# Kernel tuning notes

Measured on AMD Instinct MI355X. Metric: run time of the kernel, lower is better.

Reference implementation:

```python
import jax, jax.numpy as jnp
import numpy as np

NUM_HEADS = 8
DIM_HEAD = 64
SCALE = DIM_HEAD * NUM_HEADS  # q *= dim_head * num_heads, as in the source


def setup_inputs() -> dict:
    key = jax.random.key(0)
    k1, k2, k3, k4 = jax.random.split(key, 4)
    B, C, H, W = 8, 64, 32, 32
    x = jax.random.normal(k1, (B, C, H, W), dtype=jnp.float32)
    # 1x1 conv == matmul over channels; small init keeps post-scale logits sane
    w_qkv = jax.random.normal(k2, (3 * NUM_HEADS * DIM_HEAD, C), dtype=jnp.float32) * 0.02
    rel_h = jax.random.normal(k3, (2 * H - 1, DIM_HEAD), dtype=jnp.float32) * 0.02
    rel_w = jax.random.normal(k4, (2 * W - 1, DIM_HEAD), dtype=jnp.float32) * 0.02
    return {"x": x, "w_qkv": w_qkv, "rel_h": rel_h, "rel_w": rel_w}


def _rel_indices(H, W):
    # flattened 2D grid positions
    pos_y = np.repeat(np.arange(H), W)  # [HW]
    pos_x = np.tile(np.arange(W), H)    # [HW]
    rel_y = pos_y[None, :] - pos_y[:, None] + (H - 1)  # [HW, HW] in [0, 2H-2]
    rel_x = pos_x[None, :] - pos_x[:, None] + (W - 1)  # [HW, HW] in [0, 2W-2]
    return jnp.asarray(rel_y), jnp.asarray(rel_x)


def reference(x, w_qkv, rel_h, rel_w):
    B, C, H, W = x.shape
    n = H * W
    # 1x1 conv (bias=False) -> per-pixel matmul
    xf = x.reshape(B, C, n)                              # b c n
    qkv = jnp.einsum('oc,bcn->bon', w_qkv, xf)           # b (3 h d) n
    q, k, v = jnp.split(qkv, 3, axis=1)
    def to_heads(t):  # b (h d) n -> b h n d
        return t.reshape(B, NUM_HEADS, DIM_HEAD, n).transpose(0, 1, 3, 2)
    q, k, v = to_heads(q), to_heads(k), to_heads(v)
    q = q * SCALE  # scale applied before QK^T AND before pos bias (in-place in torch)

    sim = jnp.einsum('bhid,bhjd->bhij', q, k)            # [B, h, n, n]

    # relative position bias: q_i . rel_h[dy] + q_i . rel_w[dx]
    logits_h = jnp.einsum('bhid,rd->bhir', q, rel_h)     # [B, h, n, 2H-1]
    logits_w = jnp.einsum('bhid,rd->bhir', q, rel_w)     # [B, h, n, 2W-1]
    rel_y, rel_x = _rel_indices(H, W)                    # [n, n] each
    i_idx = jnp.arange(n)[:, None]                       # [n, 1]
    bias = logits_h[:, :, i_idx, rel_y] + logits_w[:, :, i_idx, rel_x]  # [B,h,n,n]

    attn = jax.nn.softmax(sim + bias, axis=-1)
    out = jnp.einsum('bhij,bhjd->bhid', attn, v)         # [B, h, n, d]
    out = out.transpose(0, 1, 3, 2).reshape(B, NUM_HEADS * DIM_HEAD, H, W)
    return out
```

## Files before the change

kernel.cpp:

```cpp
#include <hip/hip_runtime.h>
#include <hip/hip_bf16.h>
#include <hip/hip_fp16.h>

typedef _Float16 h8 __attribute__((ext_vector_type(8)));
typedef _Float16 h2 __attribute__((ext_vector_type(2)));
typedef unsigned short us8 __attribute__((ext_vector_type(8)));
typedef float f4 __attribute__((ext_vector_type(4)));
typedef float f16v __attribute__((ext_vector_type(16)));
typedef int i2v __attribute__((ext_vector_type(2)));

#define NH 8
#define DH 64
#define NPIX 1024
#define CIN 64
#define NBH 64
#define QSCALE (512.0f * 1.44269504f)
#define LOSCALE 2048.0f
#define INV_LOSCALE (1.0f / 2048.0f)
#define DTHR 12.0f

__device__ __forceinline__ void gload_lds16(const void* g, void* lds) {
  __builtin_amdgcn_global_load_lds(
      (const __attribute__((address_space(1))) void*)g,
      (__attribute__((address_space(3))) void*)lds, 16, 0, 0);
}

__device__ __forceinline__ float fexp2(float x) {
#if __has_builtin(__builtin_amdgcn_exp2f)
  return __builtin_amdgcn_exp2f(x);
#else
  return exp2f(x);
#endif
}

__device__ __forceinline__ unsigned pk16(float a, float b) {
  auto r = __builtin_amdgcn_cvt_pkrtz(a, b);
  union { decltype(r) h; unsigned u; } x;
  x.h = r;
  return x.u;
}

__global__ __launch_bounds__(256) void qkv_mfma(
    const float* __restrict__ x, const float* __restrict__ wqkv,
    _Float16* __restrict__ Qh, _Float16* __restrict__ Ql,
    _Float16* __restrict__ Kh, _Float16* __restrict__ Kl,
    _Float16* __restrict__ Vv) {
  __shared__ __align__(16) char QS[49152];
  char* Wh = QS;
  char* Wl = QS + 16384;
  char* Xh = QS + 32768;
  char* Xl = QS + 40960;
  char* Thi = QS;
  char* Tlo = QS + 16384;

  const int tid = threadIdx.x;
  const int lane = tid & 63;
  const int w = tid >> 6;
  const int c = lane & 15;
  const int g = lane >> 4;
  const int o0 = blockIdx.x * 128;
  const int p0 = blockIdx.y * 64;
  const int b = blockIdx.z;

  #pragma unroll
  for (int it = 0; it < 4; ++it) {
    int task = tid + it * 256;
    int oct = task & 7, o = task >> 3;
    const f4* wr = (const f4*)(wqkv + (size_t)(o0 + o) * CIN + oct * 8);
    f4 wa = wr[0], wb = wr[1];
    h8 hi, lo;
    #pragma unroll
    for (int e = 0; e < 8; ++e) {
      float v = e < 4 ? wa[e] : wb[e - 4];
      _Float16 h = (_Float16)v;
      hi[e] = h;
      lo[e] = (_Float16)((v - (float)h) * LOSCALE);
    }
    int byo = o * 128 + ((oct ^ (o & 7)) << 4);
    *(h8*)(Wh + byo) = hi;
    *(h8*)(Wl + byo) = lo;
  }
  {
    int kp = tid & 31;
    int pgrp = tid >> 5;
    const float* xr0 = x + ((size_t)b * CIN + 2 * kp) * NPIX + p0 + pgrp * 8;
    const float* xr1 = xr0 + NPIX;
    f4 a0 = *(const f4*)xr0, a1 = *(const f4*)(xr0 + 4);
    f4 b0 = *(const f4*)xr1, b1 = *(const f4*)(xr1 + 4);
    int oct = kp >> 2;
    int slot4 = (kp & 3) * 4;
    #pragma unroll
    for (int e = 0; e < 8; ++e) {
      float v0 = e < 4 ? a0[e] : a1[e - 4];
      float v1 = e < 4 ? b0[e] : b1[e - 4];
      _Float16 h0 = (_Float16)v0, h1 = (_Float16)v1;
      float l0f = (v0 - (float)h0) * LOSCALE;
      float l1f = (v1 - (float)h1) * LOSCALE;
      int p = pgrp * 8 + e;
      int byo = p * 128 + ((oct ^ (p & 7)) << 4) + slot4;
      union { h2 h; unsigned u; } uh, ul;
      uh.h[0] = h0; uh.h[1] = h1;
      ul.h[0] = (_Float16)l0f; ul.h[1] = (_Float16)l1f;
      *(unsigned*)(Xh + byo) = uh.u;
      *(unsigned*)(Xl + byo) = ul.u;
    }
  }
  __syncthreads();

  f4 zf = {0.f, 0.f, 0.f, 0.f};
  f4 acc[2][4], cor[2][4];
  #pragma unroll
  for (int oi = 0; oi < 2; ++oi)
    #pragma unroll
    for (int pi = 0; pi < 4; ++pi) { acc[oi][pi] = zf; cor[oi][pi] = zf; }

  const int ob = w * 32;
  #pragma unroll
  for (int kh = 0; kh < 2; ++kh) {
    h8 ah[2], al[2], bh[4], bl[4];
    #pragma unroll
    for (int oi = 0; oi < 2; ++oi) {
      int orow = ob + ((c >> 2) << 3) + (c & 3) + oi * 4;
      int ch = (((kh * 4 + g) ^ (orow & 7)) << 4);
      ah[oi] = *(const h8*)(Wh + orow * 128 + ch);
      al[oi] = *(const h8*)(Wl + orow * 128 + ch);
    }
    #pragma unroll
    for (int pi = 0; pi < 4; ++pi) {
      int prow = pi * 16 + c;
      int ch = (((kh * 4 + g) ^ (prow & 7)) << 4);
      bh[pi] = *(const h8*)(Xh + prow * 128 + ch);
      bl[pi] = *(const h8*)(Xl + prow * 128 + ch);
    }
    __builtin_amdgcn_s_setprio(1);
    #pragma unroll
    for (int oi = 0; oi < 2; ++oi)
      #pragma unroll
      for (int pi = 0; pi < 4; ++pi) {
        acc[oi][pi] = __builtin_amdgcn_mfma_f32_16x16x32_f16(ah[oi], bh[pi], acc[oi][pi], 0, 0, 0);
        cor[oi][pi] = __builtin_amdgcn_mfma_f32_16x16x32_f16(ah[oi], bl[pi], cor[oi][pi], 0, 0, 0);
        cor[oi][pi] = __builtin_amdgcn_mfma_f32_16x16x32_f16(al[oi], bh[pi], cor[oi][pi], 0, 0, 0);
      }
    __builtin_amdgcn_s_setprio(0);
  }

  const int part = o0 >> 9;
  const float scl = part == 0 ? QSCALE : 1.0f;
  _Float16* dsth = part == 0 ? Qh : (part == 1 ? Kh : Vv);
  _Float16* dstl = part == 0 ? Ql : (part == 1 ? Kl : nullptr);

  __syncthreads();
  {
    const int chunk = 4 * w + g;
    #pragma unroll
    for (int pi = 0; pi < 4; ++pi) {
      int p = pi * 16 + c;
      h8 hv, lv;
      #pragma unroll
      for (int oi = 0; oi < 2; ++oi)
        #pragma unroll
        for (int reg = 0; reg < 4; ++reg) {
          float v = (acc[oi][pi][reg] + cor[oi][pi][reg] * INV_LOSCALE) * scl;
          _Float16 hh = (_Float16)v;
          hv[oi * 4 + reg] = hh;
          lv[oi * 4 + reg] = (_Float16)(v - (float)hh);
        }
      int byo = p * 256 + ((chunk ^ (p & 15)) << 4);
      *(h8*)(Thi + byo) = hv;
      if (dstl) *(h8*)(Tlo + byo) = lv;
    }
  }
  __syncthreads();
  #pragma unroll
  for (int it = 0; it < 4; ++it) {
    int task = tid + it * 256;
    int p = task >> 4;
    int ck = task & 15;
    int byo = p * 256 + ((ck ^ (p & 15)) << 4);
    int o = o0 + ck * 8;
    int h = (o >> 6) & 7;
    int d = o & 63;
    size_t off = (((size_t)(b * NH + h)) * NPIX + p0 + p) * DH + d;
    h8 v = *(const h8*)(Thi + byo);
    *(h8*)(dsth + off) = v;
    if (dstl) {
      h8 v2 = *(const h8*)(Tlo + byo);
      *(h8*)(dstl + off) = v2;
    }
  }
}

__global__ __launch_bounds__(256, 2) void attn_mfma(
    const _Float16* __restrict__ Qh, const _Float16* __restrict__ Ql,
    const _Float16* __restrict__ Kh, const _Float16* __restrict__ Kl,
    const _Float16* __restrict__ V,
    const float* __restrict__ rel_h, const float* __restrict__ rel_w,
    float* __restrict__ out) {
  __shared__ __align__(16) char SMem[57344];
  _Float16* LHc = (_Float16*)(SMem + 49152);
  _Float16* LWT = (_Float16*)(SMem + 32768);
  float* OT = (float*)SMem;

  const int tid = threadIdx.x;
  const int lane = tid & 63;
  const int w = tid >> 6;
  const int wu = __builtin_amdgcn_readfirstlane(w);
  const int c = lane & 15;
  const int g = lane >> 4;
  const int il = lane & 31;
  const int hi = lane >> 5;
  const int bx = blockIdx.x;
  const int bh = ((bx & 7) << 3) | ((bx >> 3) & 7);
  const int i0 = (bx >> 6) << 7;

  const _Float16* Qhg = Qh + (size_t)bh * NPIX * DH;
  const _Float16* Qlg = Ql + (size_t)bh * NPIX * DH;
  const _Float16* Khg = Kh + (size_t)bh * NPIX * DH;
  const _Float16* Klg = Kl + (size_t)bh * NPIX * DH;
  const _Float16* Vg  = V  + (size_t)bh * NPIX * DH;

  const h8* Qr0h = (const h8*)(Qhg + (size_t)(i0 + w * 32 + c) * DH);
  const h8* Qr0l = (const h8*)(Qlg + (size_t)(i0 + w * 32 + c) * DH);
  const h8* Qr1h = (const h8*)(Qhg + (size_t)(i0 + w * 32 + 16 + c) * DH);
  const h8* Qr1l = (const h8*)(Qlg + (size_t)(i0 + w * 32 + 16 + c) * DH);
  h8 q0h[2] = {Qr0h[g], Qr0h[4 + g]};
  h8 q0l[2] = {Qr0l[g], Qr0l[4 + g]};
  h8 q1h[2] = {Qr1h[g], Qr1h[4 + g]};
  h8 q1l[2] = {Qr1l[g], Qr1l[4 + g]};

  const int s0i = wu * 128 + lane;
  const int s1i = s0i + 64;
  const int ko0 = (s0i >> 3) * 128 + (((s0i & 7) ^ ((s0i >> 3) & 7)) << 4);
  const int ko1 = (s1i >> 3) * 128 + (((s1i & 7) ^ ((s1i >> 3) & 7)) << 4);

  #pragma unroll
  for (int it = 0; it < 2; ++it) {
    int task = tid + it * 256;
    int oct = task & 7, s = task >> 3;
    int ss = s < 63 ? s : 62;
    const float* sh = rel_h + (size_t)ss * DH + oct * 8;
    const float* sw = rel_w + (size_t)ss * DH + oct * 8;
    h8 hh, ww;
    #pragma unroll
    for (int e = 0; e < 8; ++e) {
      hh[e] = (_Float16)sh[e];
      ww[e] = (_Float16)sw[e];
    }
    int byo = s * 128 + ((oct ^ (s & 7)) << 4);
    *(h8*)(SMem + byo) = hh;
    *(h8*)(SMem + 16384 + byo) = ww;
  }
  __syncthreads();

  const int yi = (i0 + w * 32) >> 5;
  f4 zf = {0.f, 0.f, 0.f, 0.f};
  #pragma unroll
  for (int rs = 0; rs < 2; ++rs) {
    f4 lhD[4], lwD[4];
    #pragma unroll
    for (int st = 0; st < 4; ++st) { lhD[st] = zf; lwD[st] = zf; }
    #pragma unroll
    for (int kh = 0; kh < 2; ++kh) {
      h8 bq = rs ? q1h[kh] : q0h[kh];
      h8 bl = rs ? q1l[kh] : q0l[kh];
      #pragma unroll
      for (int st = 0; st < 4; ++st) {
        int srow = st * 16 + c;
        int chb = srow * 128 + (((kh * 4 + g) ^ (srow & 7)) << 4);
        h8 ra = *(const h8*)(SMem + chb);
        h8 wa = *(const h8*)(SMem + 16384 + chb);
        lhD[st] = __builtin_amdgcn_mfma_f32_16x16x32_f16(ra, bq, lhD[st], 0, 0, 0);
        lhD[st] = __builtin_amdgcn_mfma_f32_16x16x32_f16(ra, bl, lhD[st], 0, 0, 0);
        lwD[st] = __builtin_amdgcn_mfma_f32_16x16x32_f16(wa, bq, lwD[st], 0, 0, 0);
        lwD[st] = __builtin_amdgcn_mfma_f32_16x16x32_f16(wa, bl, lwD[st], 0, 0, 0);
      }
    }
    int lrow = w * 32 + rs * 16 + c;
    #pragma unroll
    for (int st = 0; st < 4; ++st)
      #pragma unroll
      for (int reg = 0; reg < 4; ++reg) {
        int s = st * 16 + 4 * g + reg;
        int k = s - 31 + yi;
        if (k >= 0 && k < 32)
          LHc[(k >> 1) * 256 + lrow * 2 + (k & 1)] = (_Float16)lhD[st][reg];
        LWT[lrow * 64 + s] = (_Float16)lwD[st][reg];
      }
  }
  __syncthreads();

  float lwp[16];
  {
    int r = w * 32 + il;
    #pragma unroll
    for (int reg = 0; reg < 16; ++reg) {
      int jl = (reg & 3) + 8 * (reg >> 2) + 4 * hi;
      lwp[reg] = (float)LWT[r * 64 + 31 + jl - il];
    }
  }
  const h8* Qmh = (const h8*)(Qhg + (size_t)(i0 + w * 32 + il) * DH);
  const h8* Qml = (const h8*)(Qlg + (size_t)(i0 + w * 32 + il) * DH);
  h8 qmh[4], qml[4];
  #pragma unroll
  for (int kb = 0; kb < 4; ++kb) {
    qmh[kb] = Qmh[2 * kb + hi];
    qml[kb] = Qml[2 * kb + hi];
  }
  __syncthreads();

  {
    gload_lds16((const char*)Khg + ko0, SMem + wu * 2048);
    gload_lds16((const char*)Khg + ko1, SMem + wu * 2048 + 1024);
    gload_lds16((const char*)Klg + ko0, SMem + 16384 + wu * 2048);
    gload_lds16((const char*)Klg + ko1, SMem + 16384 + wu * 2048 + 1024);
    int jp = tid & 31, dd = tid >> 5;
    const h8* vr = (const h8*)(Vg + (size_t)(2 * jp) * DH);
    h8 v0 = vr[dd], v1 = vr[8 + dd];
    us8 u0 = *(const us8*)&v0, u1 = *(const us8*)&v1;
    #pragma unroll
    for (int e = 0; e < 8; ++e) {
      int d = dd * 8 + e;
      unsigned int val = (unsigned int)u0[e] | ((unsigned int)u1[e] << 16);
      *(unsigned int*)(SMem + 32768 + d * 128 + (((jp >> 2) ^ (d & 7)) << 4) + (jp & 3) * 4) = val;
    }
  }
  __syncthreads();

  float m_s = -1e30f, lp = 0.f;
  f16v O0, O1;
  #pragma unroll
  for (int e = 0; e < 16; ++e) { O0[e] = 0.f; O1[e] = 0.f; }

  const int swl = (il & 7);
  int cur = 0;
  #pragma unroll 1
  for (int t = 0; t < 16; ++t) {
    char* Kc  = SMem + cur * 8192;
    char* KLc = SMem + 16384 + cur * 8192;
    char* Vc  = SMem + 32768 + cur * 8192;
    const int nxt = cur ^ 1;
    const bool pre = t < 15;
    const int jp = tid & 31, dd = tid >> 5;
    h8 v0 = {}, v1 = {};
    if (pre) {
      const char* kg  = (const char*)Khg + (size_t)(t + 1) * 8192;
      const char* klg = (const char*)Klg + (size_t)(t + 1) * 8192;
      gload_lds16(kg + ko0, SMem + nxt * 8192 + wu * 2048);
      gload_lds16(kg + ko1, SMem + nxt * 8192 + wu * 2048 + 1024);
      gload_lds16(klg + ko0, SMem + 16384 + nxt * 8192 + wu * 2048);
      gload_lds16(klg + ko1, SMem + 16384 + nxt * 8192 + wu * 2048 + 1024);
      const h8* vr = (const h8*)(Vg + (size_t)((t + 1) * 64 + 2 * jp) * DH);
      v0 = vr[dd];
      v1 = vr[8 + dd];
    }

    f16v S0, S1;
    #pragma unroll
    for (int e = 0; e < 16; ++e) { S0[e] = 0.f; S1[e] = 0.f; }
    #pragma unroll
    for (int kb = 0; kb < 4; ++kb) {
      int chb0 = il * 128 + (((2 * kb + hi) ^ swl) << 4);
      int chb1 = chb0 + 32 * 128;
      h8 a0h = *(const h8*)(Kc + chb0);
      h8 a0l = *(const h8*)(KLc + chb0);
      h8 a1h = *(const h8*)(Kc + chb1);
      h8 a1l = *(const h8*)(KLc + chb1);
      __builtin_amdgcn_s_setprio(1);
      S0 = __builtin_amdgcn_mfma_f32_32x32x16_f16(a0h, qmh[kb], S0, 0, 0, 0);
      S0 = __builtin_amdgcn_mfma_f32_32x32x16_f16(a0l, qmh[kb], S0, 0, 0, 0);
      S0 = __builtin_amdgcn_mfma_f32_32x32x16_f16(a0h, qml[kb], S0, 0, 0, 0);
      S1 = __builtin_amdgcn_mfma_f32_32x32x16_f16(a1h, qmh[kb], S1, 0, 0, 0);
      S1 = __builtin_amdgcn_mfma_f32_32x32x16_f16(a1l, qmh[kb], S1, 0, 0, 0);
      S1 = __builtin_amdgcn_mfma_f32_32x32x16_f16(a1h, qml[kb], S1, 0, 0, 0);
      __builtin_amdgcn_s_setprio(0);
    }

    h8 fr[4];
    {
      int r = w * 32 + il;
      h2 lhu = *(const h2*)(LHc + t * 256 + r * 2);
      float lh0 = (float)lhu[0], lh1 = (float)lhu[1];
      #pragma unroll
      for (int reg = 0; reg < 16; ++reg) {
        S0[reg] += lwp[reg] + lh0;
        S1[reg] += lwp[reg] + lh1;
      }
      float pv0[16], pv1[16];
      #pragma unroll
      for (int e = 0; e < 16; ++e) {
        pv0[e] = fexp2(S0[e] - m_s);
        pv1[e] = fexp2(S1[e] - m_s);
      }
      float v8[8];
      #pragma unroll
      for (int e = 0; e < 8; ++e)
        v8[e] = fmaxf(fmaxf(S0[e], S0[e + 8]), fmaxf(S1[e], S1[e + 8]));
      float w0 = fmaxf(fmaxf(v8[0], v8[1]), fmaxf(v8[2], v8[3]));
      float w1 = fmaxf(fmaxf(v8[4], v8[5]), fmaxf(v8[6], v8[7]));
      float mx = fmaxf(w0, w1);
      mx = fmaxf(mx, __shfl_xor(mx, 32, 64));
      bool sk = mx <= m_s + DTHR;
      if (!__all(sk)) {
        float mn = fmaxf(m_s, mx);
        float corr = fexp2(m_s - mn);
        m_s = mn;
        lp *= corr;
        #pragma unroll
        for (int e = 0; e < 16; ++e) { O0[e] *= corr; O1[e] *= corr; }
        #pragma unroll
        for (int e = 0; e < 16; ++e) {
          pv0[e] = fexp2(S0[e] - m_s);
          pv1[e] = fexp2(S1[e] - m_s);
        }
      }
      f4 ps = zf;
      #pragma unroll
      for (int e = 0; e < 16; e += 4) {
        ps[0] += pv0[e] + pv1[e];
        ps[1] += pv0[e + 1] + pv1[e + 1];
        ps[2] += pv0[e + 2] + pv1[e + 2];
        ps[3] += pv0[e + 3] + pv1[e + 3];
      }
      lp += (ps[0] + ps[1]) + (ps[2] + ps[3]);
      #pragma unroll
      for (int jkb = 0; jkb < 4; ++jkb) {
        const float* pv = (jkb < 2) ? pv0 : pv1;
        int base = (jkb & 1) * 8;
        unsigned x01 = pk16(pv[base + 0], pv[base + 1]);
        unsigned x23 = pk16(pv[base + 2], pv[base + 3]);
        unsigned y01 = pk16(pv[base + 4], pv[base + 5]);
        unsigned y23 = pk16(pv[base + 6], pv[base + 7]);
        i2v r1 = __builtin_amdgcn_permlane32_swap((int)x01, (int)y01, false, false);
        i2v r2 = __builtin_amdgcn_permlane32_swap((int)x23, (int)y23, false, false);
        union { unsigned u[4]; h8 h; } fu;
        fu.u[0] = (unsigned)r1[0];
        fu.u[1] = (unsigned)r2[0];
        fu.u[2] = (unsigned)r1[1];
        fu.u[3] = (unsigned)r2[1];
        fr[jkb] = fu.h;
      }
    }

    #pragma unroll
    for (int jkb = 0; jkb < 4; ++jkb) {
      int och = (((2 * jkb + hi) ^ swl) << 4);
      __builtin_amdgcn_s_setprio(1);
      h8 av0 = *(const h8*)(Vc + il * 128 + och);
      h8 av1 = *(const h8*)(Vc + (32 + il) * 128 + och);
      O0 = __builtin_amdgcn_mfma_f32_32x32x16_f16(av0, fr[jkb], O0, 0, 0, 0);
      O1 = __builtin_amdgcn_mfma_f32_32x32x16_f16(av1, fr[jkb], O1, 0, 0, 0);
      __builtin_amdgcn_s_setprio(0);
    }

    if (pre) {
      us8 u0 = *(const us8*)&v0, u1 = *(const us8*)&v1;
      char* Vn = SMem + 32768 + nxt * 8192;
      #pragma unroll
      for (int e = 0; e < 8; ++e) {
        int d = dd * 8 + e;
        unsigned int val = (unsigned int)u0[e] | ((unsigned int)u1[e] << 16);
        *(unsigned int*)(Vn + d * 128 + (((jp >> 2) ^ (d & 7)) << 4) + (jp & 3) * 4) = val;
      }
    }
    __syncthreads();
    cur = nxt;
  }

  float lt = lp + __shfl_xor(lp, 32, 64);
  float rr = __builtin_amdgcn_rcpf(lt);
  {
    int r = w * 32 + il;
    #pragma unroll
    for (int reg = 0; reg < 16; ++reg) {
      int dl = (reg & 3) + 8 * (reg >> 2) + 4 * hi;
      int d0 = dl;
      int d1 = 32 + dl;
      OT[d0 * 128 + (r ^ ((d0 & 7) << 3))] = O0[reg] * rr;
      OT[d1 * 128 + (r ^ ((d1 & 7) << 3))] = O1[reg] * rr;
    }
  }
  __syncthreads();
  #pragma unroll
  for (int it = 0; it < 8; ++it) {
    int task = tid + it * 256;
    int rq = task & 31, d = task >> 5;
    f4 vv = *(const f4*)&OT[d * 128 + ((rq * 4) ^ ((d & 7) << 3))];
    *(f4*)(out + (((size_t)bh * 64 + d) << 10) + i0 + rq * 4) = vv;
  }
}

extern "C" void kernel_launch(void* const* d_in, const int* in_sizes, int n_in,
                              void* d_out, int out_size, void* d_ws, size_t ws_size,
                              hipStream_t stream) {
  const float* x  = (const float*)d_in[0];
  const float* wq = (const float*)d_in[1];
  const float* rh = (const float*)d_in[2];
  const float* rw = (const float*)d_in[3];
  float* out = (float*)d_out;

  const size_t sz = (size_t)NBH * NPIX * DH;
  _Float16* Qh = (_Float16*)d_ws;
  _Float16* Ql = Qh + sz;
  _Float16* Kh = Ql + sz;
  _Float16* Kl = Kh + sz;
  _Float16* V  = Kl + sz;

  qkv_mfma<<<dim3(12, 16, 8), 256, 0, stream>>>(x, wq, Qh, Ql, Kh, Kl, V);
  attn_mfma<<<dim3(512), 256, 0, stream>>>(Qh, Ql, Kh, Kl, V, rh, rw, out);
}
```

Measured before the change: 72.07 us.

## Store V transposed and load K/V fragments directly from global instead of LDS

```diff
diff --git a/kernel.cpp b/kernel.cpp
--- a/kernel.cpp
+++ b/kernel.cpp
@@ -4,7 +4,6 @@
 
 typedef _Float16 h8 __attribute__((ext_vector_type(8)));
 typedef _Float16 h2 __attribute__((ext_vector_type(2)));
-typedef unsigned short us8 __attribute__((ext_vector_type(8)));
 typedef float f4 __attribute__((ext_vector_type(4)));
 typedef float f16v __attribute__((ext_vector_type(16)));
 typedef int i2v __attribute__((ext_vector_type(2)));
@@ -19,12 +18,6 @@
 #define INV_LOSCALE (1.0f / 2048.0f)
 #define DTHR 12.0f
 
-__device__ __forceinline__ void gload_lds16(const void* g, void* lds) {
-  __builtin_amdgcn_global_load_lds(
-      (const __attribute__((address_space(1))) void*)g,
-      (__attribute__((address_space(3))) void*)lds, 16, 0, 0);
-}
-
 __device__ __forceinline__ float fexp2(float x) {
 #if __has_builtin(__builtin_amdgcn_exp2f)
   return __builtin_amdgcn_exp2f(x);
@@ -44,7 +37,7 @@
     const float* __restrict__ x, const float* __restrict__ wqkv,
     _Float16* __restrict__ Qh, _Float16* __restrict__ Ql,
     _Float16* __restrict__ Kh, _Float16* __restrict__ Kl,
-    _Float16* __restrict__ Vv) {
+    _Float16* __restrict__ Vt) {
   __shared__ __align__(16) char QS[49152];
   char* Wh = QS;
   char* Wl = QS + 16384;
@@ -146,7 +139,7 @@
 
   const int part = o0 >> 9;
   const float scl = part == 0 ? QSCALE : 1.0f;
-  _Float16* dsth = part == 0 ? Qh : (part == 1 ? Kh : Vv);
+  _Float16* dsth = part == 0 ? Qh : (part == 1 ? Kh : Vt);
   _Float16* dstl = part == 0 ? Ql : (part == 1 ? Kl : nullptr);
 
   __syncthreads();
@@ -171,40 +164,59 @@
     }
   }
   __syncthreads();
-  #pragma unroll
-  for (int it = 0; it < 4; ++it) {
-    int task = tid + it * 256;
-    int p = task >> 4;
-    int ck = task & 15;
-    int byo = p * 256 + ((ck ^ (p & 15)) << 4);
-    int o = o0 + ck * 8;
-    int h = (o >> 6) & 7;
-    int d = o & 63;
-    size_t off = (((size_t)(b * NH + h)) * NPIX + p0 + p) * DH + d;
-    h8 v = *(const h8*)(Thi + byo);
-    *(h8*)(dsth + off) = v;
-    if (dstl) {
-      h8 v2 = *(const h8*)(Tlo + byo);
-      *(h8*)(dstl + off) = v2;
+  if (part != 2) {
+    #pragma unroll
+    for (int it = 0; it < 4; ++it) {
+      int task = tid + it * 256;
+      int p = task >> 4;
+      int ck = task & 15;
+      int byo = p * 256 + ((ck ^ (p & 15)) << 4);
+      int o = o0 + ck * 8;
+      int h = (o >> 6) & 7;
+      int d = o & 63;
+      size_t off = (((size_t)(b * NH + h)) * NPIX + p0 + p) * DH + d;
+      h8 v = *(const h8*)(Thi + byo);
+      *(h8*)(dsth + off) = v;
+      if (dstl) {
+        h8 v2 = *(const h8*)(Tlo + byo);
+        *(h8*)(dstl + off) = v2;
+      }
+    }
+  } else {
+    #pragma unroll
+    for (int it = 0; it < 4; ++it) {
+      int task = tid + it * 256;
+      int o = task >> 3;
+      int po = task & 7;
+      h8 vv;
+      #pragma unroll
+      for (int e = 0; e < 8; ++e) {
+        int p = po * 8 + e;
+        vv[e] = *(const _Float16*)(Thi + p * 256 + (((o >> 3) ^ (p & 15)) << 4) + (o & 7) * 2);
+      }
+      int oabs = o0 + o;
+      int h = (oabs >> 6) & 7;
+      int d = oabs & 63;
+      size_t off = (((size_t)(b * NH + h)) * DH + d) * NPIX + p0 + po * 8;
+      *(h8*)(Vt + off) = vv;
     }
   }
 }
 
-__global__ __launch_bounds__(256, 2) void attn_mfma(
+__global__ __launch_bounds__(256) void attn_mfma(
     const _Float16* __restrict__ Qh, const _Float16* __restrict__ Ql,
     const _Float16* __restrict__ Kh, const _Float16* __restrict__ Kl,
-    const _Float16* __restrict__ V,
+    const _Float16* __restrict__ Vt,
     const float* __restrict__ rel_h, const float* __restrict__ rel_w,
     float* __restrict__ out) {
-  __shared__ __align__(16) char SMem[57344];
-  _Float16* LHc = (_Float16*)(SMem + 49152);
-  _Float16* LWT = (_Float16*)(SMem + 32768);
+  __shared__ __align__(16) char SMem[40960];
+  _Float16* LHc = (_Float16*)(SMem + 32768);
+  _Float16* LWT = (_Float16*)(SMem + 16384);
   float* OT = (float*)SMem;
 
   const int tid = threadIdx.x;
   const int lane = tid & 63;
   const int w = tid >> 6;
-  const int wu = __builtin_amdgcn_readfirstlane(w);
   const int c = lane & 15;
   const int g = lane >> 4;
   const int il = lane & 31;
@@ -215,9 +227,9 @@
 
   const _Float16* Qhg = Qh + (size_t)bh * NPIX * DH;
   const _Float16* Qlg = Ql + (size_t)bh * NPIX * DH;
-  const _Float16* Khg = Kh + (size_t)bh * NPIX * DH;
-  const _Float16* Klg = Kl + (size_t)bh * NPIX * DH;
-  const _Float16* Vg  = V  + (size_t)bh * NPIX * DH;
+  const h8* KH8 = (const h8*)(Kh + (size_t)bh * NPIX * DH);
+  const h8* KL8 = (const h8*)(Kl + (size_t)bh * NPIX * DH);
+  const h8* VT8 = (const h8*)(Vt + (size_t)bh * DH * NPIX);
 
   const h8* Qr0h = (const h8*)(Qhg + (size_t)(i0 + w * 32 + c) * DH);
   const h8* Qr0l = (const h8*)(Qlg + (size_t)(i0 + w * 32 + c) * DH);
@@ -228,11 +240,6 @@
   h8 q1h[2] = {Qr1h[g], Qr1h[4 + g]};
   h8 q1l[2] = {Qr1l[g], Qr1l[4 + g]};
 
-  const int s0i = wu * 128 + lane;
-  const int s1i = s0i + 64;
-  const int ko0 = (s0i >> 3) * 128 + (((s0i & 7) ^ ((s0i >> 3) & 7)) << 4);
-  const int ko1 = (s1i >> 3) * 128 + (((s1i & 7) ^ ((s1i >> 3) & 7)) << 4);
-
   #pragma unroll
   for (int it = 0; it < 2; ++it) {
     int task = tid + it * 256;
@@ -248,7 +255,7 @@
     }
     int byo = s * 128 + ((oct ^ (s & 7)) << 4);
     *(h8*)(SMem + byo) = hh;
-    *(h8*)(SMem + 16384 + byo) = ww;
+    *(h8*)(SMem + 8192 + byo) = ww;
   }
   __syncthreads();
 
@@ -268,7 +275,7 @@
         int srow = st * 16 + c;
         int chb = srow * 128 + (((kh * 4 + g) ^ (srow & 7)) << 4);
         h8 ra = *(const h8*)(SMem + chb);
-        h8 wa = *(const h8*)(SMem + 16384 + chb);
+        h8 wa = *(const h8*)(SMem + 8192 + chb);
         lhD[st] = __builtin_amdgcn_mfma_f32_16x16x32_f16(ra, bq, lhD[st], 0, 0, 0);
         lhD[st] = __builtin_amdgcn_mfma_f32_16x16x32_f16(ra, bl, lhD[st], 0, 0, 0);
         lwD[st] = __builtin_amdgcn_mfma_f32_16x16x32_f16(wa, bq, lwD[st], 0, 0, 0);
@@ -308,50 +315,29 @@
   }
   __syncthreads();
 
-  {
-    gload_lds16((const char*)Khg + ko0, SMem + wu * 2048);
-    gload_lds16((const char*)Khg + ko1, SMem + wu * 2048 + 1024);
-    gload_lds16((const char*)Klg + ko0, SMem + 16384 + wu * 2048);
-    gload_lds16((const char*)Klg + ko1, SMem + 16384 + wu * 2048 + 1024);
-    int jp = tid & 31, dd = tid >> 5;
-    const h8* vr = (const h8*)(Vg + (size_t)(2 * jp) * DH);
-    h8 v0 = vr[dd], v1 = vr[8 + dd];
-    us8 u0 = *(const us8*)&v0, u1 = *(const us8*)&v1;
-    #pragma unroll
-    for (int e = 0; e < 8; ++e) {
-      int d = dd * 8 + e;
-      unsigned int val = (unsigned int)u0[e] | ((unsigned int)u1[e] << 16);
-      *(unsigned int*)(SMem + 32768 + d * 128 + (((jp >> 2) ^ (d & 7)) << 4) + (jp & 3) * 4) = val;
-    }
-  }
-  __syncthreads();
-
   float m_s = -1e30f, lp = 0.f;
   f16v O0, O1;
   #pragma unroll
   for (int e = 0; e < 16; ++e) { O0[e] = 0.f; O1[e] = 0.f; }
 
-  const int swl = (il & 7);
-  int cur = 0;
+  const int kidx0 = il * 8 + hi;
+  const int kidx1 = (32 + il) * 8 + hi;
+  const int vidx0 = il * 128 + hi;
+  const int vidx1 = (32 + il) * 128 + hi;
+  const int lhr = (w * 32 + il) * 2;
+
   #pragma unroll 1
   for (int t = 0; t < 16; ++t) {
-    char* Kc  = SMem + cur * 8192;
-    char* KLc = SMem + 16384 + cur * 8192;
-    char* Vc  = SMem + 32768 + cur * 8192;
-    const int nxt = cur ^ 1;
-    const bool pre = t < 15;
-    const int jp = tid & 31, dd = tid >> 5;
-    h8 v0 = {}, v1 = {};
-    if (pre) {
-      const char* kg  = (const char*)Khg + (size_t)(t + 1) * 8192;
-      const char* klg = (const char*)Klg + (size_t)(t + 1) * 8192;
-      gload_lds16(kg + ko0, SMem + nxt * 8192 + wu * 2048);
-      gload_lds16(kg + ko1, SMem + nxt * 8192 + wu * 2048 + 1024);
-      gload_lds16(klg + ko0, SMem + 16384 + nxt * 8192 + wu * 2048);
-      gload_lds16(klg + ko1, SMem + 16384 + nxt * 8192 + wu * 2048 + 1024);
-      const h8* vr = (const h8*)(Vg + (size_t)((t + 1) * 64 + 2 * jp) * DH);
-      v0 = vr[dd];
-      v1 = vr[8 + dd];
+    const int kt = t * 512;
+    const int vt_ = t * 8;
+
+    h8 a0h[4], a0l[4], a1h[4], a1l[4];
+    #pragma unroll
+    for (int kb = 0; kb < 4; ++kb) {
+      a0h[kb] = KH8[kt + kidx0 + 2 * kb];
+      a0l[kb] = KL8[kt + kidx0 + 2 * kb];
+      a1h[kb] = KH8[kt + kidx1 + 2 * kb];
+      a1l[kb] = KL8[kt + kidx1 + 2 * kb];
     }
 
     f16v S0, S1;
@@ -359,26 +345,26 @@
     for (int e = 0; e < 16; ++e) { S0[e] = 0.f; S1[e] = 0.f; }
     #pragma unroll
     for (int kb = 0; kb < 4; ++kb) {
-      int chb0 = il * 128 + (((2 * kb + hi) ^ swl) << 4);
-      int chb1 = chb0 + 32 * 128;
-      h8 a0h = *(const h8*)(Kc + chb0);
-      h8 a0l = *(const h8*)(KLc + chb0);
-      h8 a1h = *(const h8*)(Kc + chb1);
-      h8 a1l = *(const h8*)(KLc + chb1);
       __builtin_amdgcn_s_setprio(1);
-      S0 = __builtin_amdgcn_mfma_f32_32x32x16_f16(a0h, qmh[kb], S0, 0, 0, 0);
-      S0 = __builtin_amdgcn_mfma_f32_32x32x16_f16(a0l, qmh[kb], S0, 0, 0, 0);
-      S0 = __builtin_amdgcn_mfma_f32_32x32x16_f16(a0h, qml[kb], S0, 0, 0, 0);
-      S1 = __builtin_amdgcn_mfma_f32_32x32x16_f16(a1h, qmh[kb], S1, 0, 0, 0);
-      S1 = __builtin_amdgcn_mfma_f32_32x32x16_f16(a1l, qmh[kb], S1, 0, 0, 0);
-      S1 = __builtin_amdgcn_mfma_f32_32x32x16_f16(a1h, qml[kb], S1, 0, 0, 0);
+      S0 = __builtin_amdgcn_mfma_f32_32x32x16_f16(a0h[kb], qmh[kb], S0, 0, 0, 0);
+      S0 = __builtin_amdgcn_mfma_f32_32x32x16_f16(a0l[kb], qmh[kb], S0, 0, 0, 0);
+      S0 = __builtin_amdgcn_mfma_f32_32x32x16_f16(a0h[kb], qml[kb], S0, 0, 0, 0);
+      S1 = __builtin_amdgcn_mfma_f32_32x32x16_f16(a1h[kb], qmh[kb], S1, 0, 0, 0);
+      S1 = __builtin_amdgcn_mfma_f32_32x32x16_f16(a1l[kb], qmh[kb], S1, 0, 0, 0);
+      S1 = __builtin_amdgcn_mfma_f32_32x32x16_f16(a1h[kb], qml[kb], S1, 0, 0, 0);
       __builtin_amdgcn_s_setprio(0);
+    }
+
+    h8 av0[4], av1[4];
+    #pragma unroll
+    for (int jkb = 0; jkb < 4; ++jkb) {
+      av0[jkb] = VT8[vidx0 + vt_ + 2 * jkb];
+      av1[jkb] = VT8[vidx1 + vt_ + 2 * jkb];
     }
 
     h8 fr[4];
     {
-      int r = w * 32 + il;
-      h2 lhu = *(const h2*)(LHc + t * 256 + r * 2);
+      h2 lhu = *(const h2*)(LHc + t * 256 + lhr);
       float lh0 = (float)lhu[0], lh1 = (float)lhu[1];
       #pragma unroll
       for (int reg = 0; reg < 16; ++reg) {
@@ -443,27 +429,11 @@
 
     #pragma unroll
     for (int jkb = 0; jkb < 4; ++jkb) {
-      int och = (((2 * jkb + hi) ^ swl) << 4);
       __builtin_amdgcn_s_setprio(1);
-      h8 av0 = *(const h8*)(Vc + il * 128 + och);
-      h8 av1 = *(const h8*)(Vc + (32 + il) * 128 + och);
-      O0 = __builtin_amdgcn_mfma_f32_32x32x16_f16(av0, fr[jkb], O0, 0, 0, 0);
-      O1 = __builtin_amdgcn_mfma_f32_32x32x16_f16(av1, fr[jkb], O1, 0, 0, 0);
+      O0 = __builtin_amdgcn_mfma_f32_32x32x16_f16(av0[jkb], fr[jkb], O0, 0, 0, 0);
+      O1 = __builtin_amdgcn_mfma_f32_32x32x16_f16(av1[jkb], fr[jkb], O1, 0, 0, 0);
       __builtin_amdgcn_s_setprio(0);
     }
-
-    if (pre) {
-      us8 u0 = *(const us8*)&v0, u1 = *(const us8*)&v1;
-      char* Vn = SMem + 32768 + nxt * 8192;
-      #pragma unroll
-      for (int e = 0; e < 8; ++e) {
-        int d = dd * 8 + e;
-        unsigned int val = (unsigned int)u0[e] | ((unsigned int)u1[e] << 16);
-        *(unsigned int*)(Vn + d * 128 + (((jp >> 2) ^ (d & 7)) << 4) + (jp & 3) * 4) = val;
-      }
-    }
-    __syncthreads();
-    cur = nxt;
   }
 
   float lt = lp + __shfl_xor(lp, 32, 64);
@@ -503,8 +473,8 @@
   _Float16* Ql = Qh + sz;
   _Float16* Kh = Ql + sz;
   _Float16* Kl = Kh + sz;
-  _Float16* V  = Kl + sz;
-
-  qkv_mfma<<<dim3(12, 16, 8), 256, 0, stream>>>(x, wq, Qh, Ql, Kh, Kl, V);
-  attn_mfma<<<dim3(512), 256, 0, stream>>>(Qh, Ql, Kh, Kl, V, rh, rw, out);
+  _Float16* Vt = Kl + sz;
+
+  qkv_mfma<<<dim3(12, 16, 8), 256, 0, stream>>>(x, wq, Qh, Ql, Kh, Kl, Vt);
+  attn_mfma<<<dim3(512), 256, 0, stream>>>(Qh, Ql, Kh, Kl, Vt, rh, rw, out);
 }
```

Measured after the change: 120.4 us. 1.67x slower.
